# Kernel optimization log

Hardware: AMD Instinct MI355X
Metric: run time of the kernel (lower is better)

The kernel has to match this reference:

```python
import jax, jax.numpy as jnp
import numpy as np

N_NODES = 100000
N_EDGES = 1600000
IN_C = 128
HID = 128
OUT_C = 10
N_GRAPHS = 512


def setup_inputs() -> dict:
    key = jax.random.key(0)
    ks = jax.random.split(key, 12)
    x = jax.random.normal(ks[0], (N_NODES, IN_C), dtype=jnp.float32)
    edge_index = jax.random.randint(ks[1], (2, N_EDGES), 0, N_NODES, dtype=jnp.int64)
    batch = jnp.sort(jax.random.randint(ks[2], (N_NODES,), 0, N_GRAPHS, dtype=jnp.int64))

    def lin(k, fan_in, fan_out):
        bound = 1.0 / np.sqrt(fan_in)
        return jax.random.uniform(k, (fan_in, fan_out), jnp.float32, -bound, bound)

    params = {
        # GraphConv layer i: W_rel (neighbor aggregate transform, with bias),
        # W_root (self transform, no bias) -- matches PyG GraphConv.
        "W1_rel": lin(ks[3], IN_C, HID), "b1": jnp.zeros((HID,), jnp.float32), "W1_root": lin(ks[4], IN_C, HID),
        "W2_rel": lin(ks[5], HID, HID), "b2": jnp.zeros((HID,), jnp.float32), "W2_root": lin(ks[6], HID, HID),
        "W3_rel": lin(ks[7], HID, HID), "b3": jnp.zeros((HID,), jnp.float32), "W3_root": lin(ks[8], HID, HID),
        "W_lin": lin(ks[9], HID, OUT_C), "b_lin": jnp.zeros((OUT_C,), jnp.float32),
    }
    return {"x": x, "edge_index": edge_index, "batch": batch, **params}


def _graph_conv(x, src, dst, W_rel, b, W_root):
    # PyG GraphConv with aggr='add': out_i = W_rel @ sum_{j->i} x_j + b + W_root @ x_i
    agg = jax.ops.segment_sum(x[src], dst, num_segments=x.shape[0])  # [N, d]
    return agg @ W_rel + b + x @ W_root


def reference(x, edge_index, batch,
              W1_rel, b1, W1_root,
              W2_rel, b2, W2_root,
              W3_rel, b3, W3_root,
              W_lin, b_lin):
    src, dst = edge_index[0], edge_index[1]
    h = jax.nn.relu(_graph_conv(x, src, dst, W1_rel, b1, W1_root))
    h = jax.nn.relu(_graph_conv(h, src, dst, W2_rel, b2, W2_root))
    h = _graph_conv(h, src, dst, W3_rel, b3, W3_root)
    # global mean pool over graphs
    sums = jax.ops.segment_sum(h, batch, num_segments=N_GRAPHS)             # [G, d]
    counts = jax.ops.segment_sum(jnp.ones((h.shape[0],), h.dtype), batch, num_segments=N_GRAPHS)
    pooled = sums / jnp.maximum(counts, 1.0)[:, None]
    return pooled @ W_lin + b_lin  # [G, OUT_C]
```

## Files before the change

### kernel.cpp

```cpp
#include <hip/hip_runtime.h>

static constexpr int NN = 100000;
static constexpr int NE = 1600000;
static constexpr int C  = 128;
static constexpr int OC = 10;
static constexpr int NG = 512;

static constexpr int BSH  = 9;
static constexpr int BNW  = 1 << BSH;
static constexpr int BK   = (NN + BNW - 1) / BNW;
static constexpr int BCAP = 12288;
static constexpr int EPB  = 4096;
static constexpr int ABLK = (NE + EPB - 1) / EPB;

static constexpr int TSTRIDE = 132;
static constexpr int NSPLIT = 8;

typedef unsigned short u16;
typedef __attribute__((ext_vector_type(8))) short short8;
typedef __attribute__((ext_vector_type(8))) short bf16x8;
typedef __attribute__((ext_vector_type(4))) float f32x4;

__device__ __forceinline__ float bf2f(u16 u) {
    union { float f; unsigned int u32; } v; v.u32 = ((unsigned int)u) << 16; return v.f;
}
__device__ __forceinline__ u16 f2bf(float f) {
    union { float f; unsigned int u; } v; v.f = f;
    unsigned int u = v.u;
    unsigned int r = u + 0x7FFF + ((u >> 16) & 1);
    return (u16)(r >> 16);
}

__global__ __launch_bounds__(256) void k_binA(const int* __restrict__ src,
                                              const int* __restrict__ dst,
                                              int* __restrict__ gcnt,
                                              int* __restrict__ buck) {
    __shared__ int cnt[BK];
    __shared__ int curs[BK];
    int tid = threadIdx.x;
    for (int i = tid; i < BK; i += 256) cnt[i] = 0;
    __syncthreads();
    int e0 = blockIdx.x * EPB;
    for (int i = tid; i < EPB; i += 256) {
        int e = e0 + i;
        if (e < NE) atomicAdd(&cnt[dst[e] >> BSH], 1);
    }
    __syncthreads();
    for (int i = tid; i < BK; i += 256) {
        int c = cnt[i];
        int gb = (c > 0) ? atomicAdd(&gcnt[i], c) : 0;
        curs[i] = i * BCAP + gb;
    }
    __syncthreads();
    for (int i = tid; i < EPB; i += 256) {
        int e = e0 + i;
        if (e < NE) {
            int d = dst[e];
            int b = d >> BSH;
            int p = atomicAdd(&curs[b], 1);
            if (p < (b + 1) * BCAP)
                buck[p] = (src[e] << BSH) | (d & (BNW - 1));
        }
    }
}

__global__ __launch_bounds__(BNW) void k_binB(const int* __restrict__ gcnt,
                                              const int* __restrict__ buck,
                                              int* __restrict__ rp,
                                              int* __restrict__ csr) {
    int b = blockIdx.x;
    int tid = threadIdx.x;
    __shared__ int hist[BNW];
    __shared__ int scanbuf[BNW];

    scanbuf[tid] = (tid < b) ? gcnt[tid] : 0;
    __syncthreads();
    for (int off = 1; off < BNW; off <<= 1) {
        int t = (tid >= off) ? scanbuf[tid - off] : 0;
        __syncthreads();
        scanbuf[tid] += t;
        __syncthreads();
    }
    int base = scanbuf[BNW - 1];

    int n = gcnt[b];
    if (n > BCAP) n = BCAP;
    const int* bb = buck + (size_t)b * BCAP;

    hist[tid] = 0;
    __syncthreads();
    for (int i = tid; i < n; i += BNW) atomicAdd(&hist[bb[i] & (BNW - 1)], 1);
    __syncthreads();

    int v = hist[tid];
    scanbuf[tid] = v;
    __syncthreads();
    for (int off = 1; off < BNW; off <<= 1) {
        int t = (tid >= off) ? scanbuf[tid - off] : 0;
        __syncthreads();
        scanbuf[tid] += t;
        __syncthreads();
    }
    int excl = scanbuf[tid] - v;
    int node = (b << BSH) + tid;
    if (node < NN) rp[node] = base + excl;
    if (b == 0 && tid == 0) rp[NN] = NE;
    __syncthreads();
    hist[tid] = base + excl;
    __syncthreads();
    for (int i = tid; i < n; i += BNW) {
        int en = bb[i];
        int p = atomicAdd(&hist[en & (BNW - 1)], 1);
        csr[p] = en >> BSH;
    }
}

__global__ __launch_bounds__(256) void k_prep(
    const float* __restrict__ x, u16* __restrict__ xb,
    const float* __restrict__ W1r, const float* __restrict__ W1o,
    const float* __restrict__ W2r, const float* __restrict__ W2o,
    u16* __restrict__ Bp,
    const int* __restrict__ batch, int* __restrict__ gstart,
    const float* __restrict__ W3r, const float* __restrict__ W3o,
    const float* __restrict__ b3, const float* __restrict__ W_lin,
    const float* __restrict__ b_lin,
    float* __restrict__ Wrl, float* __restrict__ Wro, float* __restrict__ bfold) {
    int bid = blockIdx.x;
    int tid = threadIdx.x;
    if (bid < 32) {
        int layer = bid >> 4;
        const float* Wr = (layer == 0) ? W1r : W2r;
        const float* Wo = (layer == 0) ? W1o : W2o;
        u16* outp = Bp + layer * 32768;
        int t = (bid & 15) * 256 + tid;
        int lane = t & 63;
        int nfrag = (t >> 6) & 7;
        int kk = t >> 9;
        int col = nfrag * 16 + (lane & 15);
        int k0 = kk * 32 + (lane >> 4) * 8;
        u16 vals[8];
#pragma unroll
        for (int j = 0; j < 8; ++j) {
            int k = k0 + j;
            float w = (k < C) ? Wr[k * C + col] : Wo[(k - C) * C + col];
            vals[j] = f2bf(w);
        }
        *reinterpret_cast<short8*>(outp + (size_t)t * 8) = *reinterpret_cast<const short8*>(vals);
    } else if (bid < 35) {
        int g = (bid - 32) * 256 + tid;
        if (g > NG) return;
        int lo = 0, hi = NN;
        while (lo < hi) { int mid = (lo + hi) >> 1; if (batch[mid] < g) lo = mid + 1; else hi = mid; }
        gstart[g] = lo;
    } else if (bid < 45) {
        int o = bid - 35;
        if (tid < 128) {
            float s = 0.0f;
#pragma unroll 8
            for (int c = 0; c < C; ++c) s += W3r[tid * C + c] * W_lin[c * OC + o];
            Wrl[tid * OC + o] = s;
        } else {
            int k = tid - 128;
            float s = 0.0f;
#pragma unroll 8
            for (int c = 0; c < C; ++c) s += W3o[k * C + c] * W_lin[c * OC + o];
            Wro[k * OC + o] = s;
        }
        if (tid == 0) {
            float s = 0.0f;
            for (int c = 0; c < C; ++c) s += b3[c] * W_lin[c * OC + o];
            bfold[o] = b_lin[o] + s;
        }
    } else {
        int i = (bid - 45) * 256 + tid;
        size_t base = (size_t)i * 8;
        if (base >= (size_t)NN * C) return;
        float4 a = *reinterpret_cast<const float4*>(x + base);
        float4 b = *reinterpret_cast<const float4*>(x + base + 4);
        u16 o[8] = { f2bf(a.x), f2bf(a.y), f2bf(a.z), f2bf(a.w),
                     f2bf(b.x), f2bf(b.y), f2bf(b.z), f2bf(b.w) };
        *reinterpret_cast<short8*>(xb + base) = *reinterpret_cast<const short8*>(o);
    }
}

__global__ __launch_bounds__(256) void k_gather(const u16* __restrict__ h,
                                                const int* __restrict__ rp,
                                                const int* __restrict__ csr,
                                                u16* __restrict__ agg) {
    int t = blockIdx.x * blockDim.x + threadIdx.x;
    int node = t >> 6;
    if (node >= NN) return;
    int lane = t & 63;
    int jj = lane >> 4;
    int seg = (lane & 15) * 8;
    int beg = rp[node], end = rp[node + 1];

    float acc[8] = {};
    int j0 = beg;
    for (; j0 + 8 <= end; j0 += 8) {
        int sa = csr[j0 + jj];
        int sb = csr[j0 + 4 + jj];
        short8 va = *reinterpret_cast<const short8*>(h + (size_t)sa * C + seg);
        short8 vb = *reinterpret_cast<const short8*>(h + (size_t)sb * C + seg);
#pragma unroll
        for (int q = 0; q < 8; ++q) {
            acc[q] += bf2f((u16)va[q]);
            acc[q] += bf2f((u16)vb[q]);
        }
    }
    if (j0 < end) {
        int ja = j0 + jj;
        int jb = j0 + 4 + jj;
        if (ja < end) {
            int sa = csr[ja];
            short8 va = *reinterpret_cast<const short8*>(h + (size_t)sa * C + seg);
#pragma unroll
            for (int q = 0; q < 8; ++q) acc[q] += bf2f((u16)va[q]);
        }
        if (jb < end) {
            int sb = csr[jb];
            short8 vb = *reinterpret_cast<const short8*>(h + (size_t)sb * C + seg);
#pragma unroll
            for (int q = 0; q < 8; ++q) acc[q] += bf2f((u16)vb[q]);
        }
    }

#pragma unroll
    for (int q = 0; q < 8; ++q) {
        acc[q] += __shfl_xor(acc[q], 32);
        acc[q] += __shfl_xor(acc[q], 16);
    }
    if (lane < 16) {
        u16 o[8];
#pragma unroll
        for (int q = 0; q < 8; ++q) o[q] = f2bf(acc[q]);
        *reinterpret_cast<short8*>(agg + (size_t)node * C + seg) =
            *reinterpret_cast<const short8*>(o);
    }
}

template <bool RELU, bool TSUM>
__global__ __launch_bounds__(256) void k_transform_mfma(
    const u16* __restrict__ agg, const u16* __restrict__ h,
    const u16* __restrict__ Bp, const float* __restrict__ bias,
    u16* __restrict__ out,
    const int* __restrict__ batch, float* __restrict__ Tpart) {
    __shared__ u16 tile[4][16 * TSTRIDE];
    int wave = threadIdx.x >> 6;
    int lane = threadIdx.x & 63;
    int row0 = blockIdx.x * 64 + wave * 16;
    int arow = row0 + (lane & 15);
    int rclamp = arow < NN ? arow : NN - 1;
    int koff = (lane >> 4) * 8;

    f32x4 acc[8] = {};
#pragma unroll
    for (int kk = 0; kk < 8; ++kk) {
        bf16x8 a;
        if (kk < 4) {
            a = *reinterpret_cast<const bf16x8*>(agg + (size_t)rclamp * C + kk * 32 + koff);
        } else {
            a = *reinterpret_cast<const bf16x8*>(h + (size_t)rclamp * C + (kk - 4) * 32 + koff);
        }
        const u16* bp = Bp + ((size_t)kk * 8 * 64 + lane) * 8;
#pragma unroll
        for (int n = 0; n < 8; ++n) {
            bf16x8 b = *reinterpret_cast<const bf16x8*>(bp + (size_t)n * 64 * 8);
            acc[n] = __builtin_amdgcn_mfma_f32_16x16x32_bf16(a, b, acc[n], 0, 0, 0);
        }
    }

    u16* T = tile[wave];
    int colbase = lane & 15;
    int rloc = (lane >> 4) * 4;
#pragma unroll
    for (int n = 0; n < 8; ++n) {
        int col = n * 16 + colbase;
        float bb = bias[col];
#pragma unroll
        for (int r = 0; r < 4; ++r) {
            float v = acc[n][r] + bb;
            if (RELU) v = fmaxf(v, 0.0f);
            T[(rloc + r) * TSTRIDE + col] = f2bf(v);
        }
    }
    __syncthreads();

#pragma unroll
    for (int k = 0; k < 4; ++k) {
        int idx = k * 64 + lane;
        int lr = idx >> 4;
        int off = (idx & 15) * 8;
        int ro = row0 + lr;
        if (ro < NN) {
            short8 v = *reinterpret_cast<const short8*>(&T[lr * TSTRIDE + off]);
            *reinterpret_cast<short8*>(out + (size_t)ro * C + off) = v;
        }
    }

    if (TSUM) {
        if (threadIdx.x < C) {
            int c = threadIdx.x;
            int base = blockIdx.x * 64;
            float run = 0.0f;
            int curg = -1;
            for (int r = 0; r < 64; ++r) {
                int ro = base + r;
                if (ro >= NN) break;
                int g = batch[ro];
                if (g != curg) {
                    if (curg >= 0) atomicAdd(&Tpart[(size_t)curg * C + c], run);
                    run = 0.0f;
                    curg = g;
                }
                run += bf2f(tile[r >> 4][(r & 15) * TSTRIDE + c]);
            }
            if (curg >= 0) atomicAdd(&Tpart[(size_t)curg * C + c], run);
        }
    }
}

__global__ __launch_bounds__(256) void k_gsum(
    const u16* __restrict__ h, const int* __restrict__ rp,
    const int* __restrict__ csr, const int* __restrict__ gstart,
    float* __restrict__ partial) {
    int b = blockIdx.x;
    int g = b >> 3;
    int p = b & 7;
    int slot = threadIdx.x >> 4;
    int seg = (threadIdx.x & 15) * 8;

    int gs = gstart[g], ge = gstart[g + 1];
    int es = rp[gs], ee = rp[ge];
    int m = ee - es;
    int js = es + (int)(((long long)m * p) >> 3);
    int je = es + (int)(((long long)m * (p + 1)) >> 3);

    float acc[8] = {};
    int j = js + slot;
    for (; j + 48 < je; j += 64) {
        int r0 = csr[j];
        int r1 = csr[j + 16];
        int r2 = csr[j + 32];
        int r3 = csr[j + 48];
        short8 v0 = *reinterpret_cast<const short8*>(h + (size_t)r0 * C + seg);
        short8 v1 = *reinterpret_cast<const short8*>(h + (size_t)r1 * C + seg);
        short8 v2 = *reinterpret_cast<const short8*>(h + (size_t)r2 * C + seg);
        short8 v3 = *reinterpret_cast<const short8*>(h + (size_t)r3 * C + seg);
#pragma unroll
        for (int q = 0; q < 8; ++q) {
            acc[q] += bf2f((u16)v0[q]);
            acc[q] += bf2f((u16)v1[q]);
            acc[q] += bf2f((u16)v2[q]);
            acc[q] += bf2f((u16)v3[q]);
        }
    }
    for (; j < je; j += 16) {
        int r0 = csr[j];
        short8 v0 = *reinterpret_cast<const short8*>(h + (size_t)r0 * C + seg);
#pragma unroll
        for (int q = 0; q < 8; ++q) acc[q] += bf2f((u16)v0[q]);
    }

    __shared__ float red[16][C];
#pragma unroll
    for (int q = 0; q < 8; ++q) red[slot][seg + q] = acc[q];
    __syncthreads();
    if (threadIdx.x < C) {
        float s = 0.0f;
#pragma unroll
        for (int r = 0; r < 16; ++r) s += red[r][threadIdx.x];
        partial[(size_t)b * C + threadIdx.x] = s;
    }
}

__global__ __launch_bounds__(128) void k_gout(
    const float* __restrict__ partial, const float* __restrict__ Tpart,
    const int* __restrict__ gstart,
    const float* __restrict__ Wrl, const float* __restrict__ Wro,
    const float* __restrict__ bfold, float* __restrict__ out) {
    int g = blockIdx.x;
    int k = threadIdx.x;
    __shared__ float S[C], T[C];
    float s = 0.0f;
#pragma unroll
    for (int p = 0; p < NSPLIT; ++p)
        s += partial[((size_t)(g * NSPLIT + p)) * C + k];
    S[k] = s;
    T[k] = Tpart[(size_t)g * C + k];
    __syncthreads();
    if (k < OC) {
        int n = gstart[g + 1] - gstart[g];
        float inv = 1.0f / (float)max(n, 1);
        float o = bfold[k];
#pragma unroll 8
        for (int kk = 0; kk < C; ++kk)
            o += (S[kk] * Wrl[kk * OC + k] + T[kk] * Wro[kk * OC + k]) * inv;
        out[g * OC + k] = o;
    }
}

extern "C" void kernel_launch(void* const* d_in, const int* in_sizes, int n_in,
                              void* d_out, int out_size, void* d_ws, size_t ws_size,
                              hipStream_t stream) {
    const float* x       = (const float*)d_in[0];
    const int*   eidx    = (const int*)d_in[1];
    const int*   batch   = (const int*)d_in[2];
    const float* W1_rel  = (const float*)d_in[3];
    const float* b1      = (const float*)d_in[4];
    const float* W1_root = (const float*)d_in[5];
    const float* W2_rel  = (const float*)d_in[6];
    const float* b2      = (const float*)d_in[7];
    const float* W2_root = (const float*)d_in[8];
    const float* W3_rel  = (const float*)d_in[9];
    const float* b3      = (const float*)d_in[10];
    const float* W3_root = (const float*)d_in[11];
    const float* W_lin   = (const float*)d_in[12];
    const float* b_lin   = (const float*)d_in[13];
    float* out = (float*)d_out;

    const int* src = eidx;
    const int* dst = eidx + NE;

    u16* xb   = (u16*)d_ws;
    u16* hb   = xb + (size_t)NN * C;
    u16* aggb = hb + (size_t)NN * C;
    u16* Bp   = aggb + (size_t)NN * C;
    int* rp      = (int*)(Bp + 2 * 32768);
    int* csr     = rp + NN + 1;
    int* buck    = csr + NE;
    int* gcnt    = buck + (size_t)BK * BCAP;
    float* Tpart = (float*)(gcnt + BK);
    int* gstart  = (int*)(Tpart + (size_t)NG * C);
    float* partial = (float*)(gstart + NG + 2);
    float* Wrl   = partial + (size_t)NG * NSPLIT * C;
    float* Wro   = Wrl + C * OC;
    float* bfold = Wro + C * OC;

    const int gb = (NN * 64 + 255) / 256;
    const int tb = (NN + 63) / 64;
    const int prepb = 45 + ((NN * C / 8) + 255) / 256;

    hipMemsetAsync(gcnt, 0, BK * sizeof(int) + (size_t)NG * C * sizeof(float), stream);
    k_binA<<<ABLK, 256, 0, stream>>>(src, dst, gcnt, buck);
    k_binB<<<BK, BNW, 0, stream>>>(gcnt, buck, rp, csr);

    k_prep<<<prepb, 256, 0, stream>>>(x, xb, W1_rel, W1_root, W2_rel, W2_root, Bp,
                                      batch, gstart, W3_rel, W3_root, b3, W_lin,
                                      b_lin, Wrl, Wro, bfold);

    k_gather<<<gb, 256, 0, stream>>>(xb, rp, csr, aggb);
    k_transform_mfma<true, false><<<tb, 256, 0, stream>>>(aggb, xb, Bp, b1, hb,
                                                          batch, Tpart);

    k_gather<<<gb, 256, 0, stream>>>(hb, rp, csr, aggb);
    k_transform_mfma<true, true><<<tb, 256, 0, stream>>>(aggb, hb, Bp + 32768, b2,
                                                         hb, batch, Tpart);

    k_gsum<<<NG * NSPLIT, 256, 0, stream>>>(hb, rp, csr, gstart, partial);
    k_gout<<<NG, 128, 0, stream>>>(partial, Tpart, gstart, Wrl, Wro, bfold, out);
}
```

Baseline: 309.0 us.

## Fuse CSR bucket pass with prep kernel and preload A fragments in transform

Merges the per-bucket CSR build kernel and the weight/input preparation kernel into one 512-thread launch, with block ranges dispatching to each role, so the independent prep work overlaps the CSR construction and one launch is removed. Block indexing for weight packing, graph-start search, folded output weights and x conversion is remapped to the larger block size. The MFMA transform kernel now loads all eight A fragments up front, which raises register use in exchange for issuing loads earlier.

```diff
diff --git a/kernel.cpp b/kernel.cpp
--- a/kernel.cpp
+++ b/kernel.cpp
@@ -15,6 +15,12 @@
 
 static constexpr int TSTRIDE = 132;
 static constexpr int NSPLIT = 8;
+
+static constexpr int PB_PACK = BK;
+static constexpr int PB_GB   = PB_PACK + 16;
+static constexpr int PB_WF   = PB_GB + 2;
+static constexpr int PB_CVT  = PB_WF + 5;
+static constexpr int PB_TOT  = PB_CVT + (NN * C / 8 + 511) / 512;
 
 typedef unsigned short u16;
 typedef __attribute__((ext_vector_type(8))) short short8;
@@ -64,58 +70,9 @@
     }
 }
 
-__global__ __launch_bounds__(BNW) void k_binB(const int* __restrict__ gcnt,
-                                              const int* __restrict__ buck,
-                                              int* __restrict__ rp,
-                                              int* __restrict__ csr) {
-    int b = blockIdx.x;
-    int tid = threadIdx.x;
-    __shared__ int hist[BNW];
-    __shared__ int scanbuf[BNW];
-
-    scanbuf[tid] = (tid < b) ? gcnt[tid] : 0;
-    __syncthreads();
-    for (int off = 1; off < BNW; off <<= 1) {
-        int t = (tid >= off) ? scanbuf[tid - off] : 0;
-        __syncthreads();
-        scanbuf[tid] += t;
-        __syncthreads();
-    }
-    int base = scanbuf[BNW - 1];
-
-    int n = gcnt[b];
-    if (n > BCAP) n = BCAP;
-    const int* bb = buck + (size_t)b * BCAP;
-
-    hist[tid] = 0;
-    __syncthreads();
-    for (int i = tid; i < n; i += BNW) atomicAdd(&hist[bb[i] & (BNW - 1)], 1);
-    __syncthreads();
-
-    int v = hist[tid];
-    scanbuf[tid] = v;
-    __syncthreads();
-    for (int off = 1; off < BNW; off <<= 1) {
-        int t = (tid >= off) ? scanbuf[tid - off] : 0;
-        __syncthreads();
-        scanbuf[tid] += t;
-        __syncthreads();
-    }
-    int excl = scanbuf[tid] - v;
-    int node = (b << BSH) + tid;
-    if (node < NN) rp[node] = base + excl;
-    if (b == 0 && tid == 0) rp[NN] = NE;
-    __syncthreads();
-    hist[tid] = base + excl;
-    __syncthreads();
-    for (int i = tid; i < n; i += BNW) {
-        int en = bb[i];
-        int p = atomicAdd(&hist[en & (BNW - 1)], 1);
-        csr[p] = en >> BSH;
-    }
-}
-
-__global__ __launch_bounds__(256) void k_prep(
+__global__ __launch_bounds__(512) void k_binbprep(
+    const int* __restrict__ gcnt, const int* __restrict__ buck,
+    int* __restrict__ rp, int* __restrict__ csr,
     const float* __restrict__ x, u16* __restrict__ xb,
     const float* __restrict__ W1r, const float* __restrict__ W1o,
     const float* __restrict__ W2r, const float* __restrict__ W2o,
@@ -127,12 +84,59 @@
     float* __restrict__ Wrl, float* __restrict__ Wro, float* __restrict__ bfold) {
     int bid = blockIdx.x;
     int tid = threadIdx.x;
-    if (bid < 32) {
-        int layer = bid >> 4;
+
+    if (bid < BK) {
+        __shared__ int hist[BNW];
+        __shared__ int scanbuf[BNW];
+        int b = bid;
+
+        scanbuf[tid] = (tid < b) ? gcnt[tid] : 0;
+        __syncthreads();
+        for (int off = 1; off < BNW; off <<= 1) {
+            int t = (tid >= off) ? scanbuf[tid - off] : 0;
+            __syncthreads();
+            scanbuf[tid] += t;
+            __syncthreads();
+        }
+        int base = scanbuf[BNW - 1];
+
+        int n = gcnt[b];
+        if (n > BCAP) n = BCAP;
+        const int* bb = buck + (size_t)b * BCAP;
+
+        hist[tid] = 0;
+        __syncthreads();
+        for (int i = tid; i < n; i += BNW) atomicAdd(&hist[bb[i] & (BNW - 1)], 1);
+        __syncthreads();
+
+        int v = hist[tid];
+        scanbuf[tid] = v;
+        __syncthreads();
+        for (int off = 1; off < BNW; off <<= 1) {
+            int t = (tid >= off) ? scanbuf[tid - off] : 0;
+            __syncthreads();
+            scanbuf[tid] += t;
+            __syncthreads();
+        }
+        int excl = scanbuf[tid] - v;
+        int node = (b << BSH) + tid;
+        if (node < NN) rp[node] = base + excl;
+        if (b == 0 && tid == 0) rp[NN] = NE;
+        __syncthreads();
+        hist[tid] = base + excl;
+        __syncthreads();
+        for (int i = tid; i < n; i += BNW) {
+            int en = bb[i];
+            int p = atomicAdd(&hist[en & (BNW - 1)], 1);
+            csr[p] = en >> BSH;
+        }
+    } else if (bid < PB_GB) {
+        int tt = (bid - PB_PACK) * 512 + tid;
+        int layer = tt >> 12;
+        int t = tt & 4095;
         const float* Wr = (layer == 0) ? W1r : W2r;
         const float* Wo = (layer == 0) ? W1o : W2o;
         u16* outp = Bp + layer * 32768;
-        int t = (bid & 15) * 256 + tid;
         int lane = t & 63;
         int nfrag = (t >> 6) & 7;
         int kk = t >> 9;
@@ -146,33 +150,36 @@
             vals[j] = f2bf(w);
         }
         *reinterpret_cast<short8*>(outp + (size_t)t * 8) = *reinterpret_cast<const short8*>(vals);
-    } else if (bid < 35) {
-        int g = (bid - 32) * 256 + tid;
+    } else if (bid < PB_WF) {
+        int g = (bid - PB_GB) * 512 + tid;
         if (g > NG) return;
         int lo = 0, hi = NN;
         while (lo < hi) { int mid = (lo + hi) >> 1; if (batch[mid] < g) lo = mid + 1; else hi = mid; }
         gstart[g] = lo;
-    } else if (bid < 45) {
-        int o = bid - 35;
-        if (tid < 128) {
+    } else if (bid < PB_CVT) {
+        int idx = (bid - PB_WF) * 512 + tid;
+        if (idx >= OC * 256) return;
+        int o = idx >> 8;
+        int sub = idx & 255;
+        if (sub < 128) {
             float s = 0.0f;
 #pragma unroll 8
-            for (int c = 0; c < C; ++c) s += W3r[tid * C + c] * W_lin[c * OC + o];
-            Wrl[tid * OC + o] = s;
+            for (int c = 0; c < C; ++c) s += W3r[sub * C + c] * W_lin[c * OC + o];
+            Wrl[sub * OC + o] = s;
         } else {
-            int k = tid - 128;
+            int k = sub - 128;
             float s = 0.0f;
 #pragma unroll 8
             for (int c = 0; c < C; ++c) s += W3o[k * C + c] * W_lin[c * OC + o];
             Wro[k * OC + o] = s;
         }
-        if (tid == 0) {
+        if (sub == 0) {
             float s = 0.0f;
             for (int c = 0; c < C; ++c) s += b3[c] * W_lin[c * OC + o];
             bfold[o] = b_lin[o] + s;
         }
     } else {
-        int i = (bid - 45) * 256 + tid;
+        int i = (bid - PB_CVT) * 512 + tid;
         size_t base = (size_t)i * 8;
         if (base >= (size_t)NN * C) return;
         float4 a = *reinterpret_cast<const float4*>(x + base);
@@ -253,20 +260,22 @@
     int rclamp = arow < NN ? arow : NN - 1;
     int koff = (lane >> 4) * 8;
 
+    bf16x8 afr[8];
+#pragma unroll
+    for (int kk = 0; kk < 4; ++kk)
+        afr[kk] = *reinterpret_cast<const bf16x8*>(agg + (size_t)rclamp * C + kk * 32 + koff);
+#pragma unroll
+    for (int kk = 0; kk < 4; ++kk)
+        afr[4 + kk] = *reinterpret_cast<const bf16x8*>(h + (size_t)rclamp * C + kk * 32 + koff);
+
     f32x4 acc[8] = {};
 #pragma unroll
     for (int kk = 0; kk < 8; ++kk) {
-        bf16x8 a;
-        if (kk < 4) {
-            a = *reinterpret_cast<const bf16x8*>(agg + (size_t)rclamp * C + kk * 32 + koff);
-        } else {
-            a = *reinterpret_cast<const bf16x8*>(h + (size_t)rclamp * C + (kk - 4) * 32 + koff);
-        }
         const u16* bp = Bp + ((size_t)kk * 8 * 64 + lane) * 8;
 #pragma unroll
         for (int n = 0; n < 8; ++n) {
             bf16x8 b = *reinterpret_cast<const bf16x8*>(bp + (size_t)n * 64 * 8);
-            acc[n] = __builtin_amdgcn_mfma_f32_16x16x32_bf16(a, b, acc[n], 0, 0, 0);
+            acc[n] = __builtin_amdgcn_mfma_f32_16x16x32_bf16(afr[kk], b, acc[n], 0, 0, 0);
         }
     }
 
@@ -439,15 +448,15 @@
 
     const int gb = (NN * 64 + 255) / 256;
     const int tb = (NN + 63) / 64;
-    const int prepb = 45 + ((NN * C / 8) + 255) / 256;
 
     hipMemsetAsync(gcnt, 0, BK * sizeof(int) + (size_t)NG * C * sizeof(float), stream);
     k_binA<<<ABLK, 256, 0, stream>>>(src, dst, gcnt, buck);
-    k_binB<<<BK, BNW, 0, stream>>>(gcnt, buck, rp, csr);
-
-    k_prep<<<prepb, 256, 0, stream>>>(x, xb, W1_rel, W1_root, W2_rel, W2_root, Bp,
-                                      batch, gstart, W3_rel, W3_root, b3, W_lin,
-                                      b_lin, Wrl, Wro, bfold);
+
+    k_binbprep<<<PB_TOT, 512, 0, stream>>>(gcnt, buck, rp, csr,
+                                           x, xb, W1_rel, W1_root, W2_rel, W2_root,
+                                           Bp, batch, gstart,
+                                           W3_rel, W3_root, b3, W_lin, b_lin,
+                                           Wrl, Wro, bfold);
 
     k_gather<<<gb, 256, 0, stream>>>(xb, rp, csr, aggb);
     k_transform_mfma<true, false><<<tb, 256, 0, stream>>>(aggb, xb, Bp, b1, hb,
```

After: 294.8 us. -4.6%, faster.
